# Kernel optimization log

Hardware: AMD Instinct MI355X
Metric: run time of the kernel (lower is better)

## Reference

```python
import jax, jax.numpy as jnp
import numpy as np

ALPHA = 0.2          # LeakyReLU negative slope
N = 4096             # num nodes
E = 262144           # num edges (avg degree 64)
NFEAT = 512
NHID = 64
NHEAD = 8
NCLASS = 16
NEG_INF = -1e20


def setup_inputs() -> dict:
    key = jax.random.key(0)
    ks = jax.random.split(key, 8)
    features = jax.random.normal(ks[0], (N, NFEAT), dtype=jnp.float32)
    edge_list = jax.random.randint(ks[1], (2, E), 0, N, dtype=jnp.int64)
    # xavier-uniform-ish init scaled like gain=1.414
    W_heads = jax.random.normal(ks[2], (NHEAD, NFEAT, NHID), dtype=jnp.float32) * (1.414 / np.sqrt(NFEAT))
    a_heads = jax.random.normal(ks[3], (NHEAD, 2 * NHID, 1), dtype=jnp.float32) * 0.1
    b_heads = jnp.zeros((NHEAD, NHID), dtype=jnp.float32)
    W_out = jax.random.normal(ks[4], (NHEAD * NHID, NCLASS), dtype=jnp.float32) * (1.414 / np.sqrt(NHEAD * NHID))
    a_out = jax.random.normal(ks[5], (2 * NCLASS, 1), dtype=jnp.float32) * 0.1
    b_out = jnp.zeros((NCLASS,), dtype=jnp.float32)
    return {
        "features": features, "edge_list": edge_list,
        "W_heads": W_heads, "a_heads": a_heads, "b_heads": b_heads,
        "W_out": W_out, "a_out": a_out, "b_out": b_out,
    }


def _gatconv(x, src, tgt, W, a, b):
    # dropout layers are identity in eval mode
    h = x @ W                                             # [N, F_out]
    # edge scores: gather endpoints, concat, project, LeakyReLU
    a_input = jnp.concatenate([h[src], h[tgt]], axis=1)   # [E, 2*F_out]
    e = jax.nn.leaky_relu((a_input @ a)[:, 0], ALPHA)     # [E]
    n = h.shape[0]
    # dense NxN attention: -1e20 default, edge scores scattered in
    att = jnp.full((n, n), NEG_INF, dtype=h.dtype).at[src, tgt].set(e)
    att = jax.nn.softmax(att, axis=1)                     # rows w/o edges -> uniform (matches torch)
    return att @ h + b                                    # [N, F_out]


def reference(features, edge_list, W_heads, a_heads, b_heads, W_out, a_out, b_out):
    src, tgt = edge_list[0], edge_list[1]
    # multi-head GATConv, heads vmapped over stacked params -> [H, N, NHID]
    heads = jax.vmap(lambda W, a, b: _gatconv(features, src, tgt, W, a, b))(
        W_heads, a_heads, b_heads)
    # torch.cat over heads on dim=1 == transpose+reshape
    x = jnp.transpose(heads, (1, 0, 2)).reshape(N, NHEAD * NHID)
    x = jax.nn.elu(x)
    out = _gatconv(x, src, tgt, W_out, a_out, b_out)      # [N, NCLASS]
    return jax.nn.log_softmax(out, axis=1)
```

## Files before the change

### kernel.cpp

```cpp
#include <hip/hip_runtime.h>
#include <hip/hip_bf16.h>

#define NN 4096
#define NFEAT 512
#define NHID 64
#define NHEAD 8
#define NCLASS 16
#define CAP 160
#define LALPHA 0.2f

#define SZ2 (NHEAD*2*NHID)
#define SZ3 (NHEAD*NHID)
#define SZ4 (NFEAT*NCLASS)
#define SZ5 (2*NCLASS)
#define SZ6 (NCLASS)
#define NSMALL (SZ2+SZ3+SZ4+SZ5+SZ6)
#define NGB 128

typedef __attribute__((ext_vector_type(8))) short bf16x8;
typedef __attribute__((ext_vector_type(4))) float f32x4;
typedef __attribute__((ext_vector_type(8))) unsigned short u16x8;

__device__ __forceinline__ float b2f(unsigned short h) {
    return __uint_as_float(((unsigned int)h) << 16);
}
__device__ __forceinline__ unsigned short f2b(float f) {
    unsigned int u = __float_as_uint(f);
    unsigned int r = (u + 0x7fffu + ((u >> 16) & 1u)) >> 16;
    return (unsigned short)r;
}
__device__ __forceinline__ float waveMax(float v) {
#pragma unroll
    for (int m = 32; m >= 1; m >>= 1) v = fmaxf(v, __shfl_xor(v, m, 64));
    return v;
}
__device__ __forceinline__ float waveSum(float v) {
#pragma unroll
    for (int m = 32; m >= 1; m >>= 1) v += __shfl_xor(v, m, 64);
    return v;
}
__device__ __forceinline__ float lrelu(float e) {
    return e >= 0.f ? e : LALPHA * e;
}

// ... 166 lines not shown
#pragma unroll
            for (int rh = 0; rh < 2; ++rh)
#pragma unroll
                for (int r = 0; r < 4; ++r) {
                    p1[rh][r] += __shfl_xor(p1[rh][r], m, 64);
                    p2[rh][r] += __shfl_xor(p2[rh][r], m, 64);
                }
        if (l16 == 0) {
#pragma unroll
            for (int rh = 0; rh < 2; ++rh)
#pragma unroll
                for (int r = 0; r < 4; ++r) {
                    int row = m0 + rh * 16 + quad * 4 + r;
                    s1[(h << 12) + row] = p1[rh][r];
                    s2[(h << 12) + row] = p2[rh][r];
                }
        }
        __syncthreads();
        if (t < 64) atomicAdd(&cm1[h * NHID + t], cms[t]);
        __syncthreads();
    }
}

__global__ void __launch_bounds__(256, 4)
k23(const unsigned int* __restrict__ bits,
    const float* __restrict__ s1, const float* __restrict__ s2,
    const unsigned short* __restrict__ Hb,
    const float* __restrict__ bh, const float* __restrict__ cm1,
    const float* __restrict__ Wo, const float* __restrict__ ao,
    const float* __restrict__ bo,
    float* __restrict__ out2, float* __restrict__ s1o,
    float* __restrict__ s2o, float* __restrict__ cm2,
    float* __restrict__ outp, int* __restrict__ gb) {
    __shared__ float sW[4][CAP * 8];
    __shared__ int   sT[4][CAP];
    __shared__ float cms[NCLASS];
    __shared__ float o2s[4][16];
    int t = threadIdx.x, bid = blockIdx.x, nblk = gridDim.x;
    if (t < NCLASS) cms[t] = 0.f;
    int wid = t >> 6, lane = t & 63;
    int n = bid * 4 + wid;
    int d;
    {
        uint2 w2 = *(const uint2*)&bits[n * 128 + lane * 2];
        int c = __popc(w2.x) + __popc(w2.y);
        int incl = c;
#pragma unroll
        for (int off = 1; off < 64; off <<= 1) {
            int u = __shfl_up(incl, off, 64);
            if (lane >= off) incl += u;
        }
        int excl = incl - c;
        int total = __shfl(incl, 63, 64);
        int tbase = lane * 64;
        unsigned int x = w2.x;
        while (x) {
            int b = __ffs(x) - 1; x &= x - 1;
            if (excl < CAP) sT[wid][excl] = tbase + b;
            ++excl;
        }
        unsigned int y = w2.y;
        while (y) {
            int b = __ffs(y) - 1; y &= y - 1;
            if (excl < CAP) sT[wid][excl] = tbase + 32 + b;
            ++excl;
        }
        d = min(total, CAP);
    }
    __syncthreads();
    int h = lane >> 3, jslot = lane & 7;
    float acc[8] = {};
    float rden = 1.f;
    if (d > 0) {
        const float* s2h = s2 + ((size_t)h << 12);
        float s1n = s1[(h << 12) + n];
        float mx = -1e30f;
        for (int jb = 0; jb < d; jb += 8) {
            int j = jb + jslot;
            int tt = (j < d) ? sT[wid][j] : 0;
            float e = (j < d) ? lrelu(s1n + s2h[tt]) : -1e30f;
            sW[wid][(j << 3) + h] = e;
            mx = fmaxf(mx, e);
        }
        mx = fmaxf(mx, __shfl_xor(mx, 1, 64));
        mx = fmaxf(mx, __shfl_xor(mx, 2, 64));
        mx = fmaxf(mx, __shfl_xor(mx, 4, 64));
        float den = 0.f;
        for (int jb = 0; jb < d; jb += 8) {
            int j = jb + jslot;
            float e = sW[wid][(j << 3) + h];
            float w = __expf(e - mx);
            sW[wid][(j << 3) + h] = w;
            den += w;
        }
        den += __shfl_xor(den, 1, 64);
        den += __shfl_xor(den, 2, 64);
        den += __shfl_xor(den, 4, 64);
        rden = 1.f / den;
        const unsigned short* Hp = Hb + lane * 8;
        int j = 0;
        for (; j + 4 <= d; j += 4) {
            int t0 = sT[wid][j],     t1 = sT[wid][j + 1];
            int t2 = sT[wid][j + 2], t3 = sT[wid][j + 3];
            float w0 = sW[wid][(j << 3) + h];
            float w1 = sW[wid][((j + 1) << 3) + h];
            float w2 = sW[wid][((j + 2) << 3) + h];
            float w3 = sW[wid][((j + 3) << 3) + h];
            u16x8 v0 = *(const u16x8*)(Hp + ((size_t)t0 << 9));
            u16x8 v1 = *(const u16x8*)(Hp + ((size_t)t1 << 9));
            u16x8 v2 = *(const u16x8*)(Hp + ((size_t)t2 << 9));
            u16x8 v3 = *(const u16x8*)(Hp + ((size_t)t3 << 9));
#pragma unroll
            for (int i = 0; i < 8; ++i)
                acc[i] += w0 * b2f(v0[i]) + w1 * b2f(v1[i])
                        + w2 * b2f(v2[i]) + w3 * b2f(v3[i]);
        }
        for (; j < d; ++j) {
            int t0 = sT[wid][j];
            float w0 = sW[wid][(j << 3) + h];
            u16x8 v0 = *(const u16x8*)(Hp + ((size_t)t0 << 9));
#pragma unroll
            for (int i = 0; i < 8; ++i) acc[i] += w0 * b2f(v0[i]);
        }
    }
    float o[8];
    if (d == 0) {
#pragma unroll
        for (int i = 0; i < 8; ++i) o[i] = cm1[lane * 8 + i] * (1.0f / NN);
    } else {
#pragma unroll
        for (int i = 0; i < 8; ++i) o[i] = acc[i] * rden;
    }
#pragma unroll
    for (int i = 0; i < 8; ++i) {
        float v = o[i] + bh[lane * 8 + i];
        o[i] = v > 0.f ? v : __expf(v) - 1.f;
    }
    float* xw = sW[wid];
    *(float4*)&xw[lane * 8]     = make_float4(o[0], o[1], o[2], o[3]);
    *(float4*)&xw[lane * 8 + 4] = make_float4(o[4], o[5], o[6], o[7]);
    int c = lane & 15, sub = lane >> 4;
    const float* xp = xw + sub * 128;
    const float* wp = Wo + sub * 128 * NCLASS + c;
    float a2 = 0.f;
#pragma unroll 8
    for (int kk = 0; kk < 128; ++kk) a2 += xp[kk] * wp[kk * NCLASS];
    a2 += __shfl_xor(a2, 16, 64);
    a2 += __shfl_xor(a2, 32, 64);
    if (lane < 16) out2[n * NCLASS + c] = a2;
    float r1 = a2 * ao[c], r2 = a2 * ao[NCLASS + c];
#pragma unroll
    for (int m = 8; m >= 1; m >>= 1) {
        r1 += __shfl_xor(r1, m, 16);
        r2 += __shfl_xor(r2, m, 16);
    }
    if (lane == 0) { s1o[n] = r1; s2o[n] = r2; }
    if (lane < 16) atomicAdd(&cms[c], a2);
    __syncthreads();
    if (t < NCLASS) atomicAdd(&cm2[t], cms[t]);

    gbar(gb, 1, nblk);

    {
        float val;
        if (d == 0) {
            val = cm2[c] * (1.0f / NN);
        } else {
            float s1n = s1o[n];
            float* wvw = sW[wid];
            int t0 = (lane < d)       ? sT[wid][lane]       : 0;
            int t1 = (lane + 64 < d)  ? sT[wid][lane + 64]  : 0;
            int t2 = (lane + 128 < d) ? sT[wid][lane + 128] : 0;
            float e0 = (lane < d)       ? lrelu(s1n + s2o[t0]) : -1e30f;
            float e1 = (lane + 64 < d)  ? lrelu(s1n + s2o[t1]) : -1e30f;
            float e2 = (lane + 128 < d) ? lrelu(s1n + s2o[t2]) : -1e30f;
            float m = waveMax(fmaxf(e0, fmaxf(e1, e2)));
            float w0 = (lane < d)       ? __expf(e0 - m) : 0.f;
            float w1 = (lane + 64 < d)  ? __expf(e1 - m) : 0.f;
            float w2 = (lane + 128 < d) ? __expf(e2 - m) : 0.f;
            float den = waveSum(w0 + w1 + w2);
            wvw[lane] = w0;
            wvw[lane + 64] = w1;
            if (lane + 128 < CAP) wvw[lane + 128] = w2;
            int g2 = lane >> 2, q = lane & 3;
            float a4[4] = {};
            for (int j = g2; j < d; j += 16) {
                float w = wvw[j];
                int tt = sT[wid][j];
                float4 v = *(const float4*)(out2 + tt * NCLASS + q * 4);
                a4[0] += w * v.x; a4[1] += w * v.y;
                a4[2] += w * v.z; a4[3] += w * v.w;
            }
#pragma unroll
            for (int m2 = 4; m2 <= 32; m2 <<= 1)
#pragma unroll
                for (int i = 0; i < 4; ++i) a4[i] += __shfl_xor(a4[i], m2, 64);
            if (lane < 4)
                *(float4*)&o2s[wid][lane * 4] = make_float4(a4[0], a4[1], a4[2], a4[3]);
            val = o2s[wid][c] / den;
        }
        val += bo[c];
        float mx = val;
#pragma unroll
        for (int m = 8; m >= 1; m >>= 1) mx = fmaxf(mx, __shfl_xor(mx, m, 16));
        float se = __expf(val - mx);
#pragma unroll
        for (int m = 8; m >= 1; m >>= 1) se += __shfl_xor(se, m, 16);
        float res = val - mx - __logf(se);
        if (lane < 16) outp[n * NCLASS + lane] = res;
    }
}

__global__ void __launch_bounds__(256)
k_prep0(const void* __restrict__ f, const void* __restrict__ Wh_,
        const void* __restrict__ ah_, const void* __restrict__ bh_,
        const void* __restrict__ Wo_, const void* __restrict__ ao_,
        const void* __restrict__ bo_,
        unsigned short* __restrict__ featb,
        unsigned short* __restrict__ Wtb,
        float* __restrict__ smallf,
        unsigned int* __restrict__ bits,
        float* __restrict__ cmz) {
    int t = threadIdx.x, bid = blockIdx.x;
    for (int i = bid * 256 + t; i < NN * NN / 32; i += gridDim.x * 256)
        bits[i] = 0u;
    if (bid == 0)
        for (int i = t; i < NHEAD * NHID + NCLASS; i += 256) cmz[i] = 0.f;
    __shared__ int sbf;
    if (t < 64) {
        unsigned int w = ((const unsigned int*)f)[t];
        unsigned int lo = w & 0xffffu, e = (lo >> 7) & 0xffu;
        unsigned long long bal = __ballot(lo == 0u || (e >= 100u && e <= 140u));
        if (t == 0) sbf = (__popcll(bal) >= 40);
    }
    __syncthreads();
    bool bf = (sbf != 0);
    if (bid < 128) {
        __shared__ float tile[64][33];
        int h = bid >> 4, k0 = (bid & 15) * 32;
        int n = t & 63, kh = t >> 6;
#pragma unroll
        for (int i = 0; i < 8; ++i) {
            int kk = kh * 8 + i;
            int si = (h << 15) + (k0 + kk) * NHID + n;
            float v = bf ? b2f(((const unsigned short*)Wh_)[si])
                         : ((const float*)Wh_)[si];
            tile[n][kk] = v;
        }
        __syncthreads();
        int n2 = t >> 2, kk0 = (t & 3) * 8;
        u16x8 o;
#pragma unroll
        for (int i = 0; i < 8; ++i) o[i] = f2b(tile[n2][kk0 + i]);
        *(u16x8*)&Wtb[(size_t)((h << 6) + n2) * NFEAT + k0 + kk0] = o;
    } else {
        const int NF8 = NN * NFEAT / 8;
        const int TOT = NF8 + NSMALL;
        int stride = (gridDim.x - 128) * 256;
        int start = bf ? NF8 : 0;
        for (int i = start + (bid - 128) * 256 + t; i < TOT; i += stride) {
            if (i < NF8) {
                float4 lo = ((const float4*)f)[i * 2];
                float4 hi = ((const float4*)f)[i * 2 + 1];
                u16x8 o;
                o[0] = f2b(lo.x); o[1] = f2b(lo.y); o[2] = f2b(lo.z); o[3] = f2b(lo.w);
                o[4] = f2b(hi.x); o[5] = f2b(hi.y); o[6] = f2b(hi.z); o[7] = f2b(hi.w);
                *(u16x8*)&featb[i * 8] = o;
            } else {
                int r = i - NF8;
                const void* sp; int off;
                if (r < SZ2)                        { sp = ah_; off = r; }
                else if (r < SZ2 + SZ3)             { sp = bh_; off = r - SZ2; }
                else if (r < SZ2 + SZ3 + SZ4)       { sp = Wo_; off = r - SZ2 - SZ3; }
                else if (r < SZ2 + SZ3 + SZ4 + SZ5) { sp = ao_; off = r - SZ2 - SZ3 - SZ4; }
                else                                { sp = bo_; off = r - SZ2 - SZ3 - SZ4 - SZ5; }
                smallf[r] = bf ? b2f(((const unsigned short*)sp)[off])
                               : ((const float*)sp)[off];
            }
        }
    }
}

__global__ void __launch_bounds__(256)
k_gemm_or(const void* __restrict__ f,
          const unsigned short* __restrict__ featb,
          const unsigned short* __restrict__ Wtb,
          const float* __restrict__ ah,
          unsigned short* __restrict__ Hb,
          float* __restrict__ s1, float* __restrict__ s2,
          float* __restrict__ cm1,
          const int* __restrict__ e32, int E,
          unsigned int* __restrict__ bits) {
    int t = threadIdx.x;
    if (blockIdx.x >= 256) {
        __shared__ int s64f;
        if (t < 64) {
            unsigned long long bal = __ballot(e32[2 * t + 1] == 0);
            if (t == 0) s64f = (__popcll(bal) >= 48);
        }
        __syncthreads();
        int i = (blockIdx.x - 256) * 256 + t;
        if (i < E) {
            int s, tt;
            if (s64f) { s = e32[2 * i]; tt = e32[2 * (E + i)]; }
            else      { s = e32[i];     tt = e32[E + i]; }
            s &= (NN - 1); tt &= (NN - 1);
            unsigned int pos = (unsigned int)s * NN + (unsigned int)tt;
            atomicOr(&bits[pos >> 5], 1u << (pos & 31u));
        }
        return;
    }
    __shared__ int sbf;
    if (t < 64) {
        unsigned int w = ((const unsigned int*)f)[t];
        unsigned int lo = w & 0xffffu, e = (lo >> 7) & 0xffu;
        unsigned long long bal = __ballot(lo == 0u || (e >= 100u && e <= 140u));
        if (t == 0) sbf = (__popcll(bal) >= 40);
    }
    __shared__ float cms[64];
    if (t < 64) cms[t] = 0.f;
    __syncthreads();
    const unsigned short* Ab = sbf ? (const unsigned short*)f : featb;
    int w = t >> 6, l = t & 63;
    int quad = l >> 4, l16 = l & 15;
    int h = blockIdx.x >> 5;
    int m0 = (blockIdx.x & 31) * 128 + w * 32;
    f32x4 acc[2][4] = {};
    const unsigned short* a0p = Ab + (size_t)(m0 + l16) * NFEAT + quad * 8;
    const unsigned short* a1p = a0p + 16 * NFEAT;
    const unsigned short* bp  = Wtb + ((size_t)h << 15) + (size_t)l16 * NFEAT + quad * 8;
#pragma unroll 4
    for (int k0 = 0; k0 < NFEAT; k0 += 32) {
        bf16x8 a0 = *(const bf16x8*)(a0p + k0);
        bf16x8 a1 = *(const bf16x8*)(a1p + k0);
#pragma unroll
        for (int nt = 0; nt < 4; ++nt) {
            bf16x8 b = *(const bf16x8*)(bp + (size_t)nt * 16 * NFEAT + k0);
            acc[0][nt] = __builtin_amdgcn_mfma_f32_16x16x32_bf16(a0, b, acc[0][nt], 0, 0, 0);
            acc[1][nt] = __builtin_amdgcn_mfma_f32_16x16x32_bf16(a1, b, acc[1][nt], 0, 0, 0);
        }
    }
    const float* av = ah + h * 2 * NHID;
    float p1[2][4] = {}, p2[2][4] = {};
#pragma unroll
    for (int rh = 0; rh < 2; ++rh) {
#pragma unroll
        for (int nt = 0; nt < 4; ++nt) {
            int col = nt * 16 + l16;
            float av1 = av[col], av2 = av[NHID + col];
            float csum = 0.f;
#pragma unroll
            for (int r = 0; r < 4; ++r) {
                float v = acc[rh][nt][r];
                int row = m0 + rh * 16 + quad * 4 + r;
                Hb[((size_t)row << 9) + (h << 6) + col] = f2b(v);
                p1[rh][r] += v * av1;
                p2[rh][r] += v * av2;
                csum += v;
            }
            atomicAdd(&cms[col], csum);
        }
    }
#pragma unroll
    for (int m = 8; m >= 1; m >>= 1)
#pragma unroll
        for (int rh = 0; rh < 2; ++rh)
#pragma unroll
            for (int r = 0; r < 4; ++r) {
                p1[rh][r] += __shfl_xor(p1[rh][r], m, 64);
                p2[rh][r] += __shfl_xor(p2[rh][r], m, 64);
            }
    if (l16 == 0) {
#pragma unroll
        for (int rh = 0; rh < 2; ++rh)
#pragma unroll
            for (int r = 0; r < 4; ++r) {
                int row = m0 + rh * 16 + quad * 4 + r;
                s1[(h << 12) + row] = p1[rh][r];
                s2[(h << 12) + row] = p2[rh][r];
            }
    }
    __syncthreads();
    if (t < 64) atomicAdd(&cm1[h * NHID + t], cms[t]);
}

__global__ void __launch_bounds__(256)
k_eattn1(const unsigned int* __restrict__ bits,
         int* __restrict__ deg, int* __restrict__ csr,
         const float* __restrict__ s1, const float* __restrict__ s2,
         const unsigned short* __restrict__ Hb,
         const float* __restrict__ bh, const float* __restrict__ cm1,
         const float* __restrict__ Wo, const float* __restrict__ ao,
         float* __restrict__ out2, float* __restrict__ s1o,
         float* __restrict__ s2o, float* __restrict__ cm2) {
    __shared__ float sW[4][CAP * 8];
    __shared__ int   sT[4][CAP];
    __shared__ float cms[NCLASS];
    int t = threadIdx.x;
    if (t < NCLASS) cms[t] = 0.f;
    int wid = t >> 6, lane = t & 63;
    int n = blockIdx.x * 4 + wid;
    int d;
    {
        uint2 w2 = *(const uint2*)&bits[n * 128 + lane * 2];
        int c = __popc(w2.x) + __popc(w2.y);
        int incl = c;
#pragma unroll
        for (int off = 1; off < 64; off <<= 1) {
            int u = __shfl_up(incl, off, 64);
            if (lane >= off) incl += u;
        }
        int excl = incl - c;
        int total = __shfl(incl, 63, 64);
        if (lane == 0) deg[n] = total;
        int tbase = lane * 64;
        unsigned int x = w2.x;
        while (x) {
            int b = __ffs(x) - 1; x &= x - 1;
            if (excl < CAP) sT[wid][excl] = tbase + b;
            ++excl;
        }
        unsigned int y = w2.y;
        while (y) {
            int b = __ffs(y) - 1; y &= y - 1;
            if (excl < CAP) sT[wid][excl] = tbase + 32 + b;
            ++excl;
        }
        d = min(total, CAP);
    }
    __syncthreads();
    for (int k = lane; k < d; k += 64) csr[(size_t)n * CAP + k] = sT[wid][k];
    int h = lane >> 3, jslot = lane & 7;
    float acc[8] = {};
    float rden = 1.f;
    if (d > 0) {
        const float* s2h = s2 + ((size_t)h << 12);
        float s1n = s1[(h << 12) + n];
        float mx = -1e30f;
        for (int jb = 0; jb < d; jb += 8) {
            int j = jb + jslot;
            int tt = (j < d) ? sT[wid][j] : 0;
            float e = (j < d) ? lrelu(s1n + s2h[tt]) : -1e30f;
            sW[wid][(j << 3) + h] = e;
            mx = fmaxf(mx, e);
        }
        mx = fmaxf(mx, __shfl_xor(mx, 1, 64));
        mx = fmaxf(mx, __shfl_xor(mx, 2, 64));
        mx = fmaxf(mx, __shfl_xor(mx, 4, 64));
        float den = 0.f;
        for (int jb = 0; jb < d; jb += 8) {
            int j = jb + jslot;
            float e = sW[wid][(j << 3) + h];
            float w = __expf(e - mx);
            sW[wid][(j << 3) + h] = w;
            den += w;
        }
        den += __shfl_xor(den, 1, 64);
        den += __shfl_xor(den, 2, 64);
        den += __shfl_xor(den, 4, 64);
        rden = 1.f / den;
        const unsigned short* Hp = Hb + lane * 8;
        int j = 0;
        for (; j + 4 <= d; j += 4) {
            int t0 = sT[wid][j],     t1 = sT[wid][j + 1];
            int t2 = sT[wid][j + 2], t3 = sT[wid][j + 3];
            float w0 = sW[wid][(j << 3) + h];
            float w1 = sW[wid][((j + 1) << 3) + h];
            float w2 = sW[wid][((j + 2) << 3) + h];
            float w3 = sW[wid][((j + 3) << 3) + h];
            u16x8 v0 = *(const u16x8*)(Hp + ((size_t)t0 << 9));
            u16x8 v1 = *(const u16x8*)(Hp + ((size_t)t1 << 9));
            u16x8 v2 = *(const u16x8*)(Hp + ((size_t)t2 << 9));
            u16x8 v3 = *(const u16x8*)(Hp + ((size_t)t3 << 9));
#pragma unroll
            for (int i = 0; i < 8; ++i)
                acc[i] += w0 * b2f(v0[i]) + w1 * b2f(v1[i])
                        + w2 * b2f(v2[i]) + w3 * b2f(v3[i]);
        }
        for (; j < d; ++j) {
            int t0 = sT[wid][j];
            float w0 = sW[wid][(j << 3) + h];
            u16x8 v0 = *(const u16x8*)(Hp + ((size_t)t0 << 9));
#pragma unroll
            for (int i = 0; i < 8; ++i) acc[i] += w0 * b2f(v0[i]);
        }
    }
    float o[8];
    if (d == 0) {
#pragma unroll
        for (int i = 0; i < 8; ++i) o[i] = cm1[lane * 8 + i] * (1.0f / NN);
    } else {
#pragma unroll
        for (int i = 0; i < 8; ++i) o[i] = acc[i] * rden;
    }
#pragma unroll
    for (int i = 0; i < 8; ++i) {
        float v = o[i] + bh[lane * 8 + i];
        o[i] = v > 0.f ? v : __expf(v) - 1.f;
    }
    float* xw = sW[wid];
    *(float4*)&xw[lane * 8]     = make_float4(o[0], o[1], o[2], o[3]);
    *(float4*)&xw[lane * 8 + 4] = make_float4(o[4], o[5], o[6], o[7]);
    int c = lane & 15, sub = lane >> 4;
    const float* xp = xw + sub * 128;
    const float* wp = Wo + sub * 128 * NCLASS + c;
    float a2 = 0.f;
#pragma unroll 8
    for (int kk = 0; kk < 128; ++kk) a2 += xp[kk] * wp[kk * NCLASS];
    a2 += __shfl_xor(a2, 16, 64);
    a2 += __shfl_xor(a2, 32, 64);
    if (lane < 16) out2[n * NCLASS + c] = a2;
    float r1 = a2 * ao[c], r2 = a2 * ao[NCLASS + c];
#pragma unroll
    for (int m = 8; m >= 1; m >>= 1) {
        r1 += __shfl_xor(r1, m, 16);
        r2 += __shfl_xor(r2, m, 16);
    }
    if (lane == 0) { s1o[n] = r1; s2o[n] = r2; }
    if (lane < 16) atomicAdd(&cms[c], a2);
    __syncthreads();
    if (t < NCLASS) atomicAdd(&cm2[t], cms[t]);
}

__global__ void __launch_bounds__(256)
k_attn2(const int* __restrict__ deg, const int* __restrict__ csr,
        const float* __restrict__ s1o, const float* __restrict__ s2o,
        const float* __restrict__ out2, const float* __restrict__ bo,
        const float* __restrict__ cm2, float* __restrict__ outp) {
    __shared__ float wv[4][CAP];
    __shared__ float o2s[4][16];
    int wid = threadIdx.x >> 6, lane = threadIdx.x & 63;
    int n = blockIdx.x * 4 + wid;
    int c = lane & 15;
    int d = min(deg[n], CAP);
    float val;
    if (d == 0) {
        val = cm2[c] * (1.0f / NN);
    } else {
        float s1n = s1o[n];
        const int* rowp = csr + (size_t)n * CAP;
        int t0 = (lane < d)       ? rowp[lane]       : 0;
        int t1 = (lane + 64 < d)  ? rowp[lane + 64]  : 0;
// ... 17 lines not shown
            float4 v = *(const float4*)(out2 + tt * NCLASS + q * 4);
            a4[0] += w * v.x; a4[1] += w * v.y;
            a4[2] += w * v.z; a4[3] += w * v.w;
        }
#pragma unroll
        for (int m2 = 4; m2 <= 32; m2 <<= 1)
#pragma unroll
            for (int i = 0; i < 4; ++i) a4[i] += __shfl_xor(a4[i], m2, 64);
        if (lane < 4)
            *(float4*)&o2s[wid][lane * 4] = make_float4(a4[0], a4[1], a4[2], a4[3]);
        val = o2s[wid][c] / den;
    }
    val += bo[c];
    float mx = val;
#pragma unroll
    for (int m = 8; m >= 1; m >>= 1) mx = fmaxf(mx, __shfl_xor(mx, m, 16));
    float se = __expf(val - mx);
#pragma unroll
    for (int m = 8; m >= 1; m >>= 1) se += __shfl_xor(se, m, 16);
    float res = val - mx - __logf(se);
    if (lane < 16) outp[n * NCLASS + lane] = res;
}

extern "C" void kernel_launch(void* const* d_in, const int* in_sizes, int n_in,
                              void* d_out, int out_size, void* d_ws, size_t ws_size,
                              hipStream_t stream) {
    const void* features = d_in[0];
    const int*  edges    = (const int*)d_in[1];
    const void* W_heads  = d_in[2];
    const void* a_heads  = d_in[3];
    const void* b_heads  = d_in[4];
    const void* W_out    = d_in[5];
    const void* a_out    = d_in[6];
    const void* b_out    = d_in[7];
    int E = in_sizes[1] / 2;
    int csb = (E + 255) / 256;

    int*   gb   = (int*)d_ws;
    float* cm1  = (float*)(gb + NGB);
    float* cm2  = cm1 + NHEAD * NHID;
    unsigned int* bits = (unsigned int*)(cm2 + NCLASS);
    int*   deg  = (int*)(bits + (NN * NN / 32));
    int*   csr  = deg + NN;
    float* s1   = (float*)(csr + NN * CAP);
    float* s2   = s1 + NHEAD * NN;
    float* out2 = s2 + NHEAD * NN;
    float* s1o  = out2 + NN * NCLASS;
    float* s2o  = s1o + NN;
    float* smallf = s2o + NN;
    unsigned short* Hb    = (unsigned short*)(smallf + NSMALL);
    unsigned short* featb = Hb + (size_t)NN * NHEAD * NHID;
    unsigned short* Wtb   = featb + (size_t)NN * NFEAT;
    float* outp = (float*)d_out;
    const float* bhf = smallf + SZ2;
    const float* Wof = smallf + SZ2 + SZ3;
    const float* aof = Wof + SZ4;
    const float* bof = aof + SZ5;

    static int cap01 = -2, cap23 = -2;
    if (cap01 == -2) {
        int b01 = 0, b23 = 0, ncu = 0, dev = 0;
        (void)hipGetDevice(&dev);
        if (hipDeviceGetAttribute(&ncu, hipDeviceAttributeMultiprocessorCount, dev)
                != hipSuccess) ncu = 0;
        if (hipOccupancyMaxActiveBlocksPerMultiprocessor(
                &b01, reinterpret_cast<const void*>(&k01), 256, 0) != hipSuccess) b01 = 0;
        if (hipOccupancyMaxActiveBlocksPerMultiprocessor(
                &b23, reinterpret_cast<const void*>(&k23), 256, 0) != hipSuccess) b23 = 0;
        cap01 = (b01 > 0 && ncu > 0) ? b01 * ncu : 0;
        cap23 = (b23 > 0 && ncu > 0) ? b23 * ncu : 0;
    }
    int nblk01 = cap01 > 1024 ? 1024 : cap01;

    if (nblk01 >= 128 && cap23 >= NN / 4) {
        hipMemsetAsync(d_ws, 0, (size_t)(NGB + NHEAD * NHID + NCLASS) * 4, stream);
        hipLaunchKernelGGL(k01, dim3(nblk01), dim3(256), 0, stream,
                           features, W_heads, a_heads, b_heads, W_out, a_out, b_out,
                           edges, E, csb, featb, Wtb, smallf, bits, Hb, s1, s2, cm1, gb);
        hipLaunchKernelGGL(k23, dim3(NN / 4), dim3(256), 0, stream,
                           bits, s1, s2, Hb, bhf, cm1, Wof, aof, bof,
                           out2, s1o, s2o, cm2, outp, gb);
    } else {
        hipLaunchKernelGGL(k_prep0, dim3(2048), dim3(256), 0, stream,
                           features, W_heads, a_heads, b_heads, W_out, a_out, b_out,
                           featb, Wtb, smallf, bits, cm1);
        hipLaunchKernelGGL(k_gemm_or, dim3(256 + csb), dim3(256), 0, stream,
                           features, featb, Wtb, smallf, Hb, s1, s2, cm1, edges, E, bits);
        hipLaunchKernelGGL(k_eattn1, dim3(NN / 4), dim3(256), 0, stream,
                           bits, deg, csr, s1, s2, Hb, bhf, cm1, Wof, aof,
                           out2, s1o, s2o, cm2);
        hipLaunchKernelGGL(k_attn2, dim3(NN / 4), dim3(256), 0, stream,
                           deg, csr, s1o, s2o, out2, bof, cm2, outp);
    }
}
```

Measured before the change: 141.1 us.

## Replace grid-barrier attention kernel with split-head two-wave-per-node attention kernels

```diff
diff --git a/kernel.cpp b/kernel.cpp
--- a/kernel.cpp
+++ b/kernel.cpp
@@ -20,6 +20,7 @@
 typedef __attribute__((ext_vector_type(8))) short bf16x8;
 typedef __attribute__((ext_vector_type(4))) float f32x4;
 typedef __attribute__((ext_vector_type(8))) unsigned short u16x8;
+typedef __attribute__((ext_vector_type(4))) unsigned short u16x4;
 
 __device__ __forceinline__ float b2f(unsigned short h) {
     return __uint_as_float(((unsigned int)h) << 16);
@@ -232,370 +233,8 @@
     }
 }
 
-__global__ void __launch_bounds__(256, 4)
-k23(const unsigned int* __restrict__ bits,
-    const float* __restrict__ s1, const float* __restrict__ s2,
-    const unsigned short* __restrict__ Hb,
-    const float* __restrict__ bh, const float* __restrict__ cm1,
-    const float* __restrict__ Wo, const float* __restrict__ ao,
-    const float* __restrict__ bo,
-    float* __restrict__ out2, float* __restrict__ s1o,
-    float* __restrict__ s2o, float* __restrict__ cm2,
-    float* __restrict__ outp, int* __restrict__ gb) {
-    __shared__ float sW[4][CAP * 8];
-    __shared__ int   sT[4][CAP];
-    __shared__ float cms[NCLASS];
-    __shared__ float o2s[4][16];
-    int t = threadIdx.x, bid = blockIdx.x, nblk = gridDim.x;
-    if (t < NCLASS) cms[t] = 0.f;
-    int wid = t >> 6, lane = t & 63;
-    int n = bid * 4 + wid;
-    int d;
-    {
-        uint2 w2 = *(const uint2*)&bits[n * 128 + lane * 2];
-        int c = __popc(w2.x) + __popc(w2.y);
-        int incl = c;
-#pragma unroll
-        for (int off = 1; off < 64; off <<= 1) {
-            int u = __shfl_up(incl, off, 64);
-            if (lane >= off) incl += u;
-        }
-        int excl = incl - c;
-        int total = __shfl(incl, 63, 64);
-        int tbase = lane * 64;
-        unsigned int x = w2.x;
-        while (x) {
-            int b = __ffs(x) - 1; x &= x - 1;
-            if (excl < CAP) sT[wid][excl] = tbase + b;
-            ++excl;
-        }
-        unsigned int y = w2.y;
-        while (y) {
-            int b = __ffs(y) - 1; y &= y - 1;
-            if (excl < CAP) sT[wid][excl] = tbase + 32 + b;
-            ++excl;
-        }
-        d = min(total, CAP);
-    }
-    __syncthreads();
-    int h = lane >> 3, jslot = lane & 7;
-    float acc[8] = {};
-    float rden = 1.f;
-    if (d > 0) {
-        const float* s2h = s2 + ((size_t)h << 12);
-        float s1n = s1[(h << 12) + n];
-        float mx = -1e30f;
-        for (int jb = 0; jb < d; jb += 8) {
-            int j = jb + jslot;
-            int tt = (j < d) ? sT[wid][j] : 0;
-            float e = (j < d) ? lrelu(s1n + s2h[tt]) : -1e30f;
-            sW[wid][(j << 3) + h] = e;
-            mx = fmaxf(mx, e);
-        }
-        mx = fmaxf(mx, __shfl_xor(mx, 1, 64));
-        mx = fmaxf(mx, __shfl_xor(mx, 2, 64));
-        mx = fmaxf(mx, __shfl_xor(mx, 4, 64));
-        float den = 0.f;
-        for (int jb = 0; jb < d; jb += 8) {
-            int j = jb + jslot;
-            float e = sW[wid][(j << 3) + h];
-            float w = __expf(e - mx);
-            sW[wid][(j << 3) + h] = w;
-            den += w;
-        }
-        den += __shfl_xor(den, 1, 64);
-        den += __shfl_xor(den, 2, 64);
-        den += __shfl_xor(den, 4, 64);
-        rden = 1.f / den;
-        const unsigned short* Hp = Hb + lane * 8;
-        int j = 0;
-        for (; j + 4 <= d; j += 4) {
-            int t0 = sT[wid][j],     t1 = sT[wid][j + 1];
-            int t2 = sT[wid][j + 2], t3 = sT[wid][j + 3];
-            float w0 = sW[wid][(j << 3) + h];
-            float w1 = sW[wid][((j + 1) << 3) + h];
-            float w2 = sW[wid][((j + 2) << 3) + h];
-            float w3 = sW[wid][((j + 3) << 3) + h];
-            u16x8 v0 = *(const u16x8*)(Hp + ((size_t)t0 << 9));
-            u16x8 v1 = *(const u16x8*)(Hp + ((size_t)t1 << 9));
-            u16x8 v2 = *(const u16x8*)(Hp + ((size_t)t2 << 9));
-            u16x8 v3 = *(const u16x8*)(Hp + ((size_t)t3 << 9));
-#pragma unroll
-            for (int i = 0; i < 8; ++i)
-                acc[i] += w0 * b2f(v0[i]) + w1 * b2f(v1[i])
-                        + w2 * b2f(v2[i]) + w3 * b2f(v3[i]);
-        }
-        for (; j < d; ++j) {
-            int t0 = sT[wid][j];
-            float w0 = sW[wid][(j << 3) + h];
-            u16x8 v0 = *(const u16x8*)(Hp + ((size_t)t0 << 9));
-#pragma unroll
-            for (int i = 0; i < 8; ++i) acc[i] += w0 * b2f(v0[i]);
-        }
-    }
-    float o[8];
-    if (d == 0) {
-#pragma unroll
-        for (int i = 0; i < 8; ++i) o[i] = cm1[lane * 8 + i] * (1.0f / NN);
-    } else {
-#pragma unroll
-        for (int i = 0; i < 8; ++i) o[i] = acc[i] * rden;
-    }
-#pragma unroll
-    for (int i = 0; i < 8; ++i) {
-        float v = o[i] + bh[lane * 8 + i];
-        o[i] = v > 0.f ? v : __expf(v) - 1.f;
-    }
-    float* xw = sW[wid];
-    *(float4*)&xw[lane * 8]     = make_float4(o[0], o[1], o[2], o[3]);
-    *(float4*)&xw[lane * 8 + 4] = make_float4(o[4], o[5], o[6], o[7]);
-    int c = lane & 15, sub = lane >> 4;
-    const float* xp = xw + sub * 128;
-    const float* wp = Wo + sub * 128 * NCLASS + c;
-    float a2 = 0.f;
-#pragma unroll 8
-    for (int kk = 0; kk < 128; ++kk) a2 += xp[kk] * wp[kk * NCLASS];
-    a2 += __shfl_xor(a2, 16, 64);
-    a2 += __shfl_xor(a2, 32, 64);
-    if (lane < 16) out2[n * NCLASS + c] = a2;
-    float r1 = a2 * ao[c], r2 = a2 * ao[NCLASS + c];
-#pragma unroll
-    for (int m = 8; m >= 1; m >>= 1) {
-        r1 += __shfl_xor(r1, m, 16);
-        r2 += __shfl_xor(r2, m, 16);
-    }
-    if (lane == 0) { s1o[n] = r1; s2o[n] = r2; }
-    if (lane < 16) atomicAdd(&cms[c], a2);
-    __syncthreads();
-    if (t < NCLASS) atomicAdd(&cm2[t], cms[t]);
-
-    gbar(gb, 1, nblk);
-
-    {
-        float val;
-        if (d == 0) {
-            val = cm2[c] * (1.0f / NN);
-        } else {
-            float s1n = s1o[n];
-            float* wvw = sW[wid];
-            int t0 = (lane < d)       ? sT[wid][lane]       : 0;
-            int t1 = (lane + 64 < d)  ? sT[wid][lane + 64]  : 0;
-            int t2 = (lane + 128 < d) ? sT[wid][lane + 128] : 0;
-            float e0 = (lane < d)       ? lrelu(s1n + s2o[t0]) : -1e30f;
-            float e1 = (lane + 64 < d)  ? lrelu(s1n + s2o[t1]) : -1e30f;
-            float e2 = (lane + 128 < d) ? lrelu(s1n + s2o[t2]) : -1e30f;
-            float m = waveMax(fmaxf(e0, fmaxf(e1, e2)));
-            float w0 = (lane < d)       ? __expf(e0 - m) : 0.f;
-            float w1 = (lane + 64 < d)  ? __expf(e1 - m) : 0.f;
-            float w2 = (lane + 128 < d) ? __expf(e2 - m) : 0.f;
-            float den = waveSum(w0 + w1 + w2);
-            wvw[lane] = w0;
-            wvw[lane + 64] = w1;
-            if (lane + 128 < CAP) wvw[lane + 128] = w2;
-            int g2 = lane >> 2, q = lane & 3;
-            float a4[4] = {};
-            for (int j = g2; j < d; j += 16) {
-                float w = wvw[j];
-                int tt = sT[wid][j];
-                float4 v = *(const float4*)(out2 + tt * NCLASS + q * 4);
-                a4[0] += w * v.x; a4[1] += w * v.y;
-                a4[2] += w * v.z; a4[3] += w * v.w;
-            }
-#pragma unroll
-            for (int m2 = 4; m2 <= 32; m2 <<= 1)
-#pragma unroll
-                for (int i = 0; i < 4; ++i) a4[i] += __shfl_xor(a4[i], m2, 64);
-            if (lane < 4)
-                *(float4*)&o2s[wid][lane * 4] = make_float4(a4[0], a4[1], a4[2], a4[3]);
-            val = o2s[wid][c] / den;
-        }
-        val += bo[c];
-        float mx = val;
-#pragma unroll
-        for (int m = 8; m >= 1; m >>= 1) mx = fmaxf(mx, __shfl_xor(mx, m, 16));
-        float se = __expf(val - mx);
-#pragma unroll
-        for (int m = 8; m >= 1; m >>= 1) se += __shfl_xor(se, m, 16);
-        float res = val - mx - __logf(se);
-        if (lane < 16) outp[n * NCLASS + lane] = res;
-    }
-}
-
 __global__ void __launch_bounds__(256)
-k_prep0(const void* __restrict__ f, const void* __restrict__ Wh_,
-        const void* __restrict__ ah_, const void* __restrict__ bh_,
-        const void* __restrict__ Wo_, const void* __restrict__ ao_,
-        const void* __restrict__ bo_,
-        unsigned short* __restrict__ featb,
-        unsigned short* __restrict__ Wtb,
-        float* __restrict__ smallf,
-        unsigned int* __restrict__ bits,
-        float* __restrict__ cmz) {
-    int t = threadIdx.x, bid = blockIdx.x;
-    for (int i = bid * 256 + t; i < NN * NN / 32; i += gridDim.x * 256)
-        bits[i] = 0u;
-    if (bid == 0)
-        for (int i = t; i < NHEAD * NHID + NCLASS; i += 256) cmz[i] = 0.f;
-    __shared__ int sbf;
-    if (t < 64) {
-        unsigned int w = ((const unsigned int*)f)[t];
-        unsigned int lo = w & 0xffffu, e = (lo >> 7) & 0xffu;
-        unsigned long long bal = __ballot(lo == 0u || (e >= 100u && e <= 140u));
-        if (t == 0) sbf = (__popcll(bal) >= 40);
-    }
-    __syncthreads();
-    bool bf = (sbf != 0);
-    if (bid < 128) {
-        __shared__ float tile[64][33];
-        int h = bid >> 4, k0 = (bid & 15) * 32;
-        int n = t & 63, kh = t >> 6;
-#pragma unroll
-        for (int i = 0; i < 8; ++i) {
-            int kk = kh * 8 + i;
-            int si = (h << 15) + (k0 + kk) * NHID + n;
-            float v = bf ? b2f(((const unsigned short*)Wh_)[si])
-                         : ((const float*)Wh_)[si];
-            tile[n][kk] = v;
-        }
-        __syncthreads();
-        int n2 = t >> 2, kk0 = (t & 3) * 8;
-        u16x8 o;
-#pragma unroll
-        for (int i = 0; i < 8; ++i) o[i] = f2b(tile[n2][kk0 + i]);
-        *(u16x8*)&Wtb[(size_t)((h << 6) + n2) * NFEAT + k0 + kk0] = o;
-    } else {
-        const int NF8 = NN * NFEAT / 8;
-        const int TOT = NF8 + NSMALL;
-        int stride = (gridDim.x - 128) * 256;
-        int start = bf ? NF8 : 0;
-        for (int i = start + (bid - 128) * 256 + t; i < TOT; i += stride) {
-            if (i < NF8) {
-                float4 lo = ((const float4*)f)[i * 2];
-                float4 hi = ((const float4*)f)[i * 2 + 1];
-                u16x8 o;
-                o[0] = f2b(lo.x); o[1] = f2b(lo.y); o[2] = f2b(lo.z); o[3] = f2b(lo.w);
-                o[4] = f2b(hi.x); o[5] = f2b(hi.y); o[6] = f2b(hi.z); o[7] = f2b(hi.w);
-                *(u16x8*)&featb[i * 8] = o;
-            } else {
-                int r = i - NF8;
-                const void* sp; int off;
-                if (r < SZ2)                        { sp = ah_; off = r; }
-                else if (r < SZ2 + SZ3)             { sp = bh_; off = r - SZ2; }
-                else if (r < SZ2 + SZ3 + SZ4)       { sp = Wo_; off = r - SZ2 - SZ3; }
-                else if (r < SZ2 + SZ3 + SZ4 + SZ5) { sp = ao_; off = r - SZ2 - SZ3 - SZ4; }
-                else                                { sp = bo_; off = r - SZ2 - SZ3 - SZ4 - SZ5; }
-                smallf[r] = bf ? b2f(((const unsigned short*)sp)[off])
-                               : ((const float*)sp)[off];
-            }
-        }
-    }
-}
-
-__global__ void __launch_bounds__(256)
-k_gemm_or(const void* __restrict__ f,
-          const unsigned short* __restrict__ featb,
-          const unsigned short* __restrict__ Wtb,
-          const float* __restrict__ ah,
-          unsigned short* __restrict__ Hb,
-          float* __restrict__ s1, float* __restrict__ s2,
-          float* __restrict__ cm1,
-          const int* __restrict__ e32, int E,
-          unsigned int* __restrict__ bits) {
-    int t = threadIdx.x;
-    if (blockIdx.x >= 256) {
-        __shared__ int s64f;
-        if (t < 64) {
-            unsigned long long bal = __ballot(e32[2 * t + 1] == 0);
-            if (t == 0) s64f = (__popcll(bal) >= 48);
-        }
-        __syncthreads();
-        int i = (blockIdx.x - 256) * 256 + t;
-        if (i < E) {
-            int s, tt;
-            if (s64f) { s = e32[2 * i]; tt = e32[2 * (E + i)]; }
-            else      { s = e32[i];     tt = e32[E + i]; }
-            s &= (NN - 1); tt &= (NN - 1);
-            unsigned int pos = (unsigned int)s * NN + (unsigned int)tt;
-            atomicOr(&bits[pos >> 5], 1u << (pos & 31u));
-        }
-        return;
-    }
-    __shared__ int sbf;
-    if (t < 64) {
-        unsigned int w = ((const unsigned int*)f)[t];
-        unsigned int lo = w & 0xffffu, e = (lo >> 7) & 0xffu;
-        unsigned long long bal = __ballot(lo == 0u || (e >= 100u && e <= 140u));
-        if (t == 0) sbf = (__popcll(bal) >= 40);
-    }
-    __shared__ float cms[64];
-    if (t < 64) cms[t] = 0.f;
-    __syncthreads();
-    const unsigned short* Ab = sbf ? (const unsigned short*)f : featb;
-    int w = t >> 6, l = t & 63;
-    int quad = l >> 4, l16 = l & 15;
-    int h = blockIdx.x >> 5;
-    int m0 = (blockIdx.x & 31) * 128 + w * 32;
-    f32x4 acc[2][4] = {};
-    const unsigned short* a0p = Ab + (size_t)(m0 + l16) * NFEAT + quad * 8;
-    const unsigned short* a1p = a0p + 16 * NFEAT;
-    const unsigned short* bp  = Wtb + ((size_t)h << 15) + (size_t)l16 * NFEAT + quad * 8;
-#pragma unroll 4
-    for (int k0 = 0; k0 < NFEAT; k0 += 32) {
-        bf16x8 a0 = *(const bf16x8*)(a0p + k0);
-        bf16x8 a1 = *(const bf16x8*)(a1p + k0);
-#pragma unroll
-        for (int nt = 0; nt < 4; ++nt) {
-            bf16x8 b = *(const bf16x8*)(bp + (size_t)nt * 16 * NFEAT + k0);
-            acc[0][nt] = __builtin_amdgcn_mfma_f32_16x16x32_bf16(a0, b, acc[0][nt], 0, 0, 0);
-            acc[1][nt] = __builtin_amdgcn_mfma_f32_16x16x32_bf16(a1, b, acc[1][nt], 0, 0, 0);
-        }
-    }
-    const float* av = ah + h * 2 * NHID;
-    float p1[2][4] = {}, p2[2][4] = {};
-#pragma unroll
-    for (int rh = 0; rh < 2; ++rh) {
-#pragma unroll
-        for (int nt = 0; nt < 4; ++nt) {
-            int col = nt * 16 + l16;
-            float av1 = av[col], av2 = av[NHID + col];
-            float csum = 0.f;
-#pragma unroll
-            for (int r = 0; r < 4; ++r) {
-                float v = acc[rh][nt][r];
-                int row = m0 + rh * 16 + quad * 4 + r;
-                Hb[((size_t)row << 9) + (h << 6) + col] = f2b(v);
-                p1[rh][r] += v * av1;
-                p2[rh][r] += v * av2;
-                csum += v;
-            }
-            atomicAdd(&cms[col], csum);
-        }
-    }
-#pragma unroll
-    for (int m = 8; m >= 1; m >>= 1)
-#pragma unroll
-        for (int rh = 0; rh < 2; ++rh)
-#pragma unroll
-            for (int r = 0; r < 4; ++r) {
-                p1[rh][r] += __shfl_xor(p1[rh][r], m, 64);
-                p2[rh][r] += __shfl_xor(p2[rh][r], m, 64);
-            }
-    if (l16 == 0) {
-#pragma unroll
-        for (int rh = 0; rh < 2; ++rh)
-#pragma unroll
-            for (int r = 0; r < 4; ++r) {
-                int row = m0 + rh * 16 + quad * 4 + r;
-                s1[(h << 12) + row] = p1[rh][r];
-                s2[(h << 12) + row] = p2[rh][r];
-            }
-    }
-    __syncthreads();
-    if (t < 64) atomicAdd(&cm1[h * NHID + t], cms[t]);
-}
-
-__global__ void __launch_bounds__(256)
-k_eattn1(const unsigned int* __restrict__ bits,
+k_attn1h(const unsigned int* __restrict__ bits,
          int* __restrict__ deg, int* __restrict__ csr,
          const float* __restrict__ s1, const float* __restrict__ s2,
          const unsigned short* __restrict__ Hb,
@@ -603,15 +242,17 @@
          const float* __restrict__ Wo, const float* __restrict__ ao,
          float* __restrict__ out2, float* __restrict__ s1o,
          float* __restrict__ s2o, float* __restrict__ cm2) {
-    __shared__ float sW[4][CAP * 8];
-    __shared__ int   sT[4][CAP];
+    __shared__ int   sT[2][CAP];
+    __shared__ int   sDeg[2];
+    __shared__ float sW[4][CAP * 4];
+    __shared__ float xr[2][NFEAT];
     __shared__ float cms[NCLASS];
     int t = threadIdx.x;
     if (t < NCLASS) cms[t] = 0.f;
-    int wid = t >> 6, lane = t & 63;
-    int n = blockIdx.x * 4 + wid;
-    int d;
-    {
+    int w = t >> 6, lane = t & 63;
+    int nl = w >> 1, hg = w & 1;
+    int n = blockIdx.x * 2 + nl;
+    if (hg == 0) {
         uint2 w2 = *(const uint2*)&bits[n * 128 + lane * 2];
         int c = __popc(w2.x) + __popc(w2.y);
         int incl = c;
@@ -622,112 +263,118 @@
         }
         int excl = incl - c;
         int total = __shfl(incl, 63, 64);
-        if (lane == 0) deg[n] = total;
+        if (lane == 0) { deg[n] = total; sDeg[nl] = total; }
         int tbase = lane * 64;
         unsigned int x = w2.x;
         while (x) {
             int b = __ffs(x) - 1; x &= x - 1;
-            if (excl < CAP) sT[wid][excl] = tbase + b;
+            if (excl < CAP) sT[nl][excl] = tbase + b;
             ++excl;
         }
         unsigned int y = w2.y;
         while (y) {
             int b = __ffs(y) - 1; y &= y - 1;
-            if (excl < CAP) sT[wid][excl] = tbase + 32 + b;
+            if (excl < CAP) sT[nl][excl] = tbase + 32 + b;
             ++excl;
         }
-        d = min(total, CAP);
-    }
-    __syncthreads();
-    for (int k = lane; k < d; k += 64) csr[(size_t)n * CAP + k] = sT[wid][k];
-    int h = lane >> 3, jslot = lane & 7;
-    float acc[8] = {};
+    }
+    __syncthreads();
+    int d = min(sDeg[nl], CAP);
+    if (hg == 0)
+        for (int k = lane; k < d; k += 64) csr[(size_t)n * CAP + k] = sT[nl][k];
+    int hp = lane >> 4, jslot = lane & 15;
+    int h = hg * 4 + hp;
+    float acc[4] = {};
     float rden = 1.f;
     if (d > 0) {
         const float* s2h = s2 + ((size_t)h << 12);
         float s1n = s1[(h << 12) + n];
         float mx = -1e30f;
-        for (int jb = 0; jb < d; jb += 8) {
+        for (int jb = 0; jb < d; jb += 16) {
             int j = jb + jslot;
-            int tt = (j < d) ? sT[wid][j] : 0;
+            int tt = (j < d) ? sT[nl][j] : 0;
             float e = (j < d) ? lrelu(s1n + s2h[tt]) : -1e30f;
-            sW[wid][(j << 3) + h] = e;
+            sW[w][(j << 2) + hp] = e;
             mx = fmaxf(mx, e);
         }
         mx = fmaxf(mx, __shfl_xor(mx, 1, 64));
         mx = fmaxf(mx, __shfl_xor(mx, 2, 64));
         mx = fmaxf(mx, __shfl_xor(mx, 4, 64));
+        mx = fmaxf(mx, __shfl_xor(mx, 8, 64));
         float den = 0.f;
-        for (int jb = 0; jb < d; jb += 8) {
+        for (int jb = 0; jb < d; jb += 16) {
             int j = jb + jslot;
-            float e = sW[wid][(j << 3) + h];
-            float w = __expf(e - mx);
-            sW[wid][(j << 3) + h] = w;
-            den += w;
+            float e = sW[w][(j << 2) + hp];
+            float ww = __expf(e - mx);
+            sW[w][(j << 2) + hp] = ww;
+            den += ww;
         }
         den += __shfl_xor(den, 1, 64);
         den += __shfl_xor(den, 2, 64);
         den += __shfl_xor(den, 4, 64);
+        den += __shfl_xor(den, 8, 64);
         rden = 1.f / den;
-        const unsigned short* Hp = Hb + lane * 8;
+        const unsigned short* Hp = Hb + hg * 256 + lane * 4;
         int j = 0;
         for (; j + 4 <= d; j += 4) {
-            int t0 = sT[wid][j],     t1 = sT[wid][j + 1];
-            int t2 = sT[wid][j + 2], t3 = sT[wid][j + 3];
-            float w0 = sW[wid][(j << 3) + h];
-            float w1 = sW[wid][((j + 1) << 3) + h];
-            float w2 = sW[wid][((j + 2) << 3) + h];
-            float w3 = sW[wid][((j + 3) << 3) + h];
-            u16x8 v0 = *(const u16x8*)(Hp + ((size_t)t0 << 9));
-            u16x8 v1 = *(const u16x8*)(Hp + ((size_t)t1 << 9));
-            u16x8 v2 = *(const u16x8*)(Hp + ((size_t)t2 << 9));
-            u16x8 v3 = *(const u16x8*)(Hp + ((size_t)t3 << 9));
-#pragma unroll
-            for (int i = 0; i < 8; ++i)
+            int t0 = sT[nl][j],     t1 = sT[nl][j + 1];
+            int t2 = sT[nl][j + 2], t3 = sT[nl][j + 3];
+            float w0 = sW[w][(j << 2) + hp];
+            float w1 = sW[w][((j + 1) << 2) + hp];
+            float w2 = sW[w][((j + 2) << 2) + hp];
+            float w3 = sW[w][((j + 3) << 2) + hp];
+            u16x4 v0 = *(const u16x4*)(Hp + ((size_t)t0 << 9));
+            u16x4 v1 = *(const u16x4*)(Hp + ((size_t)t1 << 9));
+            u16x4 v2 = *(const u16x4*)(Hp + ((size_t)t2 << 9));
+            u16x4 v3 = *(const u16x4*)(Hp + ((size_t)t3 << 9));
+#pragma unroll
+            for (int i = 0; i < 4; ++i)
                 acc[i] += w0 * b2f(v0[i]) + w1 * b2f(v1[i])
                         + w2 * b2f(v2[i]) + w3 * b2f(v3[i]);
         }
         for (; j < d; ++j) {
-            int t0 = sT[wid][j];
-            float w0 = sW[wid][(j << 3) + h];
-            u16x8 v0 = *(const u16x8*)(Hp + ((size_t)t0 << 9));
-#pragma unroll
-            for (int i = 0; i < 8; ++i) acc[i] += w0 * b2f(v0[i]);
-        }
-    }
-    float o[8];
+            int t0 = sT[nl][j];
+            float w0 = sW[w][(j << 2) + hp];
+            u16x4 v0 = *(const u16x4*)(Hp + ((size_t)t0 << 9));
+#pragma unroll
+            for (int i = 0; i < 4; ++i) acc[i] += w0 * b2f(v0[i]);
+        }
+    }
+    float o[4];
+    int fbase = hg * 256 + lane * 4;
     if (d == 0) {
 #pragma unroll
-        for (int i = 0; i < 8; ++i) o[i] = cm1[lane * 8 + i] * (1.0f / NN);
+        for (int i = 0; i < 4; ++i) o[i] = cm1[fbase + i] * (1.0f / NN);
     } else {
 #pragma unroll
-        for (int i = 0; i < 8; ++i) o[i] = acc[i] * rden;
-    }
-#pragma unroll
-    for (int i = 0; i < 8; ++i) {
-        float v = o[i] + bh[lane * 8 + i];
+        for (int i = 0; i < 4; ++i) o[i] = acc[i] * rden;
+    }
+#pragma unroll
+    for (int i = 0; i < 4; ++i) {
+        float v = o[i] + bh[fbase + i];
         o[i] = v > 0.f ? v : __expf(v) - 1.f;
     }
-    float* xw = sW[wid];
-    *(float4*)&xw[lane * 8]     = make_float4(o[0], o[1], o[2], o[3]);
-    *(float4*)&xw[lane * 8 + 4] = make_float4(o[4], o[5], o[6], o[7]);
-    int c = lane & 15, sub = lane >> 4;
-    const float* xp = xw + sub * 128;
-    const float* wp = Wo + sub * 128 * NCLASS + c;
-    float a2 = 0.f;
+    *(float4*)&xr[nl][fbase] = make_float4(o[0], o[1], o[2], o[3]);
+    __syncthreads();
+    if (hg == 0) {
+        int c = lane & 15, sub = lane >> 4;
+        const float* xp = xr[nl] + sub * 128;
+        const float* wp = Wo + sub * 128 * NCLASS + c;
+        float a2 = 0.f;
 #pragma unroll 8
-    for (int kk = 0; kk < 128; ++kk) a2 += xp[kk] * wp[kk * NCLASS];
-    a2 += __shfl_xor(a2, 16, 64);
-    a2 += __shfl_xor(a2, 32, 64);
-    if (lane < 16) out2[n * NCLASS + c] = a2;
-    float r1 = a2 * ao[c], r2 = a2 * ao[NCLASS + c];
-#pragma unroll
-    for (int m = 8; m >= 1; m >>= 1) {
-        r1 += __shfl_xor(r1, m, 16);
-        r2 += __shfl_xor(r2, m, 16);
-    }
-    if (lane == 0) { s1o[n] = r1; s2o[n] = r2; }
-    if (lane < 16) atomicAdd(&cms[c], a2);
+        for (int kk = 0; kk < 128; ++kk) a2 += xp[kk] * wp[kk * NCLASS];
+        a2 += __shfl_xor(a2, 16, 64);
+        a2 += __shfl_xor(a2, 32, 64);
+        if (lane < 16) out2[n * NCLASS + c] = a2;
+        float r1 = a2 * ao[c], r2 = a2 * ao[NCLASS + c];
+#pragma unroll
+        for (int m = 8; m >= 1; m >>= 1) {
+            r1 += __shfl_xor(r1, m, 16);
+            r2 += __shfl_xor(r2, m, 16);
+        }
+        if (lane == 0) { s1o[n] = r1; s2o[n] = r2; }
+        if (lane < 16) atomicAdd(&cms[c], a2);
+    }
     __syncthreads();
     if (t < NCLASS) atomicAdd(&cm2[t], cms[t]);
 }
@@ -791,6 +438,179 @@
     if (lane < 16) outp[n * NCLASS + lane] = res;
 }
 
+__global__ void __launch_bounds__(256)
+k_prep0(const void* __restrict__ f, const void* __restrict__ Wh_,
+        const void* __restrict__ ah_, const void* __restrict__ bh_,
+        const void* __restrict__ Wo_, const void* __restrict__ ao_,
+        const void* __restrict__ bo_,
+        unsigned short* __restrict__ featb,
+        unsigned short* __restrict__ Wtb,
+        float* __restrict__ smallf,
+        unsigned int* __restrict__ bits,
+        float* __restrict__ cmz) {
+    int t = threadIdx.x, bid = blockIdx.x;
+    for (int i = bid * 256 + t; i < NN * NN / 32; i += gridDim.x * 256)
+        bits[i] = 0u;
+    if (bid == 0)
+        for (int i = t; i < NHEAD * NHID + NCLASS; i += 256) cmz[i] = 0.f;
+    __shared__ int sbf;
+    if (t < 64) {
+        unsigned int w = ((const unsigned int*)f)[t];
+        unsigned int lo = w & 0xffffu, e = (lo >> 7) & 0xffu;
+        unsigned long long bal = __ballot(lo == 0u || (e >= 100u && e <= 140u));
+        if (t == 0) sbf = (__popcll(bal) >= 40);
+    }
+    __syncthreads();
+    bool bf = (sbf != 0);
+    if (bid < 128) {
+        __shared__ float tile[64][33];
+        int h = bid >> 4, k0 = (bid & 15) * 32;
+        int n = t & 63, kh = t >> 6;
+#pragma unroll
+        for (int i = 0; i < 8; ++i) {
+            int kk = kh * 8 + i;
+            int si = (h << 15) + (k0 + kk) * NHID + n;
+            float v = bf ? b2f(((const unsigned short*)Wh_)[si])
+                         : ((const float*)Wh_)[si];
+            tile[n][kk] = v;
+        }
+        __syncthreads();
+        int n2 = t >> 2, kk0 = (t & 3) * 8;
+        u16x8 o;
+#pragma unroll
+        for (int i = 0; i < 8; ++i) o[i] = f2b(tile[n2][kk0 + i]);
+        *(u16x8*)&Wtb[(size_t)((h << 6) + n2) * NFEAT + k0 + kk0] = o;
+    } else {
+        const int NF8 = NN * NFEAT / 8;
+        const int TOT = NF8 + NSMALL;
+        int stride = (gridDim.x - 128) * 256;
+        int start = bf ? NF8 : 0;
+        for (int i = start + (bid - 128) * 256 + t; i < TOT; i += stride) {
+            if (i < NF8) {
+                float4 lo = ((const float4*)f)[i * 2];
+                float4 hi = ((const float4*)f)[i * 2 + 1];
+                u16x8 o;
+                o[0] = f2b(lo.x); o[1] = f2b(lo.y); o[2] = f2b(lo.z); o[3] = f2b(lo.w);
+                o[4] = f2b(hi.x); o[5] = f2b(hi.y); o[6] = f2b(hi.z); o[7] = f2b(hi.w);
+                *(u16x8*)&featb[i * 8] = o;
+            } else {
+                int r = i - NF8;
+                const void* sp; int off;
+                if (r < SZ2)                        { sp = ah_; off = r; }
+                else if (r < SZ2 + SZ3)             { sp = bh_; off = r - SZ2; }
+                else if (r < SZ2 + SZ3 + SZ4)       { sp = Wo_; off = r - SZ2 - SZ3; }
+                else if (r < SZ2 + SZ3 + SZ4 + SZ5) { sp = ao_; off = r - SZ2 - SZ3 - SZ4; }
+                else                                { sp = bo_; off = r - SZ2 - SZ3 - SZ4 - SZ5; }
+                smallf[r] = bf ? b2f(((const unsigned short*)sp)[off])
+                               : ((const float*)sp)[off];
+            }
+        }
+    }
+}
+
+__global__ void __launch_bounds__(256)
+k_gemm_or(const void* __restrict__ f,
+          const unsigned short* __restrict__ featb,
+          const unsigned short* __restrict__ Wtb,
+          const float* __restrict__ ah,
+          unsigned short* __restrict__ Hb,
+          float* __restrict__ s1, float* __restrict__ s2,
+          float* __restrict__ cm1,
+          const int* __restrict__ e32, int E,
+          unsigned int* __restrict__ bits) {
+    int t = threadIdx.x;
+    if (blockIdx.x >= 256) {
+        __shared__ int s64f;
+        if (t < 64) {
+            unsigned long long bal = __ballot(e32[2 * t + 1] == 0);
+            if (t == 0) s64f = (__popcll(bal) >= 48);
+        }
+        __syncthreads();
+        int i = (blockIdx.x - 256) * 256 + t;
+        if (i < E) {
+            int s, tt;
+            if (s64f) { s = e32[2 * i]; tt = e32[2 * (E + i)]; }
+            else      { s = e32[i];     tt = e32[E + i]; }
+            s &= (NN - 1); tt &= (NN - 1);
+            unsigned int pos = (unsigned int)s * NN + (unsigned int)tt;
+            atomicOr(&bits[pos >> 5], 1u << (pos & 31u));
+        }
+        return;
+    }
+    __shared__ int sbf;
+    if (t < 64) {
+        unsigned int w = ((const unsigned int*)f)[t];
+        unsigned int lo = w & 0xffffu, e = (lo >> 7) & 0xffu;
+        unsigned long long bal = __ballot(lo == 0u || (e >= 100u && e <= 140u));
+        if (t == 0) sbf = (__popcll(bal) >= 40);
+    }
+    __shared__ float cms[64];
+    if (t < 64) cms[t] = 0.f;
+    __syncthreads();
+    const unsigned short* Ab = sbf ? (const unsigned short*)f : featb;
+    int w = t >> 6, l = t & 63;
+    int quad = l >> 4, l16 = l & 15;
+    int h = blockIdx.x >> 5;
+    int m0 = (blockIdx.x & 31) * 128 + w * 32;
+    f32x4 acc[2][4] = {};
+    const unsigned short* a0p = Ab + (size_t)(m0 + l16) * NFEAT + quad * 8;
+    const unsigned short* a1p = a0p + 16 * NFEAT;
+    const unsigned short* bp  = Wtb + ((size_t)h << 15) + (size_t)l16 * NFEAT + quad * 8;
+#pragma unroll 4
+    for (int k0 = 0; k0 < NFEAT; k0 += 32) {
+        bf16x8 a0 = *(const bf16x8*)(a0p + k0);
+        bf16x8 a1 = *(const bf16x8*)(a1p + k0);
+#pragma unroll
+        for (int nt = 0; nt < 4; ++nt) {
+            bf16x8 b = *(const bf16x8*)(bp + (size_t)nt * 16 * NFEAT + k0);
+            acc[0][nt] = __builtin_amdgcn_mfma_f32_16x16x32_bf16(a0, b, acc[0][nt], 0, 0, 0);
+            acc[1][nt] = __builtin_amdgcn_mfma_f32_16x16x32_bf16(a1, b, acc[1][nt], 0, 0, 0);
+        }
+    }
+    const float* av = ah + h * 2 * NHID;
+    float p1[2][4] = {}, p2[2][4] = {};
+#pragma unroll
+    for (int rh = 0; rh < 2; ++rh) {
+#pragma unroll
+        for (int nt = 0; nt < 4; ++nt) {
+            int col = nt * 16 + l16;
+            float av1 = av[col], av2 = av[NHID + col];
+            float csum = 0.f;
+#pragma unroll
+            for (int r = 0; r < 4; ++r) {
+                float v = acc[rh][nt][r];
+                int row = m0 + rh * 16 + quad * 4 + r;
+                Hb[((size_t)row << 9) + (h << 6) + col] = f2b(v);
+                p1[rh][r] += v * av1;
+                p2[rh][r] += v * av2;
+                csum += v;
+            }
+            atomicAdd(&cms[col], csum);
+        }
+    }
+#pragma unroll
+    for (int m = 8; m >= 1; m >>= 1)
+#pragma unroll
+        for (int rh = 0; rh < 2; ++rh)
+#pragma unroll
+            for (int r = 0; r < 4; ++r) {
+                p1[rh][r] += __shfl_xor(p1[rh][r], m, 64);
+                p2[rh][r] += __shfl_xor(p2[rh][r], m, 64);
+            }
+    if (l16 == 0) {
+#pragma unroll
+        for (int rh = 0; rh < 2; ++rh)
+#pragma unroll
+            for (int r = 0; r < 4; ++r) {
+                int row = m0 + rh * 16 + quad * 4 + r;
+                s1[(h << 12) + row] = p1[rh][r];
+                s2[(h << 12) + row] = p2[rh][r];
+            }
+    }
+    __syncthreads();
+    if (t < 64) atomicAdd(&cm1[h * NHID + t], cms[t]);
+}
+
 extern "C" void kernel_launch(void* const* d_in, const int* in_sizes, int n_in,
                               void* d_out, int out_size, void* d_ws, size_t ws_size,
                               hipStream_t stream) {
@@ -826,39 +646,33 @@
     const float* aof = Wof + SZ4;
     const float* bof = aof + SZ5;
 
-    static int cap01 = -2, cap23 = -2;
+    static int cap01 = -2;
     if (cap01 == -2) {
-        int b01 = 0, b23 = 0, ncu = 0, dev = 0;
+        int b01 = 0, ncu = 0, dev = 0;
         (void)hipGetDevice(&dev);
         if (hipDeviceGetAttribute(&ncu, hipDeviceAttributeMultiprocessorCount, dev)
                 != hipSuccess) ncu = 0;
         if (hipOccupancyMaxActiveBlocksPerMultiprocessor(
                 &b01, reinterpret_cast<const void*>(&k01), 256, 0) != hipSuccess) b01 = 0;
-        if (hipOccupancyMaxActiveBlocksPerMultiprocessor(
-                &b23, reinterpret_cast<const void*>(&k23), 256, 0) != hipSuccess) b23 = 0;
         cap01 = (b01 > 0 && ncu > 0) ? b01 * ncu : 0;
-        cap23 = (b23 > 0 && ncu > 0) ? b23 * ncu : 0;
     }
     int nblk01 = cap01 > 1024 ? 1024 : cap01;
 
-    if (nblk01 >= 128 && cap23 >= NN / 4) {
-        hipMemsetAsync(d_ws, 0, (size_t)(NGB + NHEAD * NHID + NCLASS) * 4, stream);
+    hipMemsetAsync(d_ws, 0, (size_t)(NGB + NHEAD * NHID + NCLASS) * 4, stream);
+    if (nblk01 >= 128) {
         hipLaunchKernelGGL(k01, dim3(nblk01), dim3(256), 0, stream,
                            features, W_heads, a_heads, b_heads, W_out, a_out, b_out,
                            edges, E, csb, featb, Wtb, smallf, bits, Hb, s1, s2, cm1, gb);
-        hipLaunchKernelGGL(k23, dim3(NN / 4), dim3(256), 0, stream,
-                           bits, s1, s2, Hb, bhf, cm1, Wof, aof, bof,
-                           out2, s1o, s2o, cm2, outp, gb);
     } else {
         hipLaunchKernelGGL(k_prep0, dim3(2048), dim3(256), 0, stream,
                            features, W_heads, a_heads, b_heads, W_out, a_out, b_out,
                            featb, Wtb, smallf, bits, cm1);
         hipLaunchKernelGGL(k_gemm_or, dim3(256 + csb), dim3(256), 0, stream,
                            features, featb, Wtb, smallf, Hb, s1, s2, cm1, edges, E, bits);
-        hipLaunchKernelGGL(k_eattn1, dim3(NN / 4), dim3(256), 0, stream,
-                           bits, deg, csr, s1, s2, Hb, bhf, cm1, Wof, aof,
-                           out2, s1o, s2o, cm2);
-        hipLaunchKernelGGL(k_attn2, dim3(NN / 4), dim3(256), 0, stream,
-                           deg, csr, s1o, s2o, out2, bof, cm2, outp);
-    }
-}
+    }
+    hipLaunchKernelGGL(k_attn1h, dim3(NN / 2), dim3(256), 0, stream,
+                       bits, deg, csr, s1, s2, Hb, bhf, cm1, Wof, aof,
+                       out2, s1o, s2o, cm2);
+    hipLaunchKernelGGL(k_attn2, dim3(NN / 4), dim3(256), 0, stream,
+                       deg, csr, s1o, s2o, out2, bof, cm2, outp);
+}
```

Measured after the change: 190.9 us. 35.2% more time.
